# Optimization experiments

Hardware: AMD Instinct MI355X
Metric: run time of the kernel (lower is better)

## Reference

```python
import jax, jax.numpy as jnp
import numpy as np

H = W = 9
C = 16
D = 34
NHEAD = 2
HDIM = D // NHEAD  # 17
FF = 2048
NLAYERS = 2
EPS = 1e-5


def setup_inputs() -> dict:
    key = jax.random.key(0)
    ks = jax.random.split(key, 16)
    s = 0.05
    return {
        "obs": jax.random.normal(ks[0], (2, H, W), dtype=jnp.float32),
        "conv1_w": jax.random.normal(ks[1], (16, 2, 3, 3), dtype=jnp.float32) * s,
        "conv1_b": jnp.zeros((16,), jnp.float32),
        "conv2_w": jax.random.normal(ks[2], (16, 16, 3, 3), dtype=jnp.float32) * s,
        "conv2_b": jnp.zeros((16,), jnp.float32),
        "in_proj_w": jax.random.normal(ks[3], (NLAYERS, 3 * D, D), dtype=jnp.float32) * s,
        "in_proj_b": jnp.zeros((NLAYERS, 3 * D), jnp.float32),
        "out_proj_w": jax.random.normal(ks[4], (NLAYERS, D, D), dtype=jnp.float32) * s,
        "out_proj_b": jnp.zeros((NLAYERS, D), jnp.float32),
        "lin1_w": jax.random.normal(ks[5], (NLAYERS, FF, D), dtype=jnp.float32) * s,
        "lin1_b": jnp.zeros((NLAYERS, FF), jnp.float32),
        "lin2_w": jax.random.normal(ks[6], (NLAYERS, D, FF), dtype=jnp.float32) * s,
        "lin2_b": jnp.zeros((NLAYERS, D), jnp.float32),
        "ln1_g": jnp.ones((NLAYERS, D), jnp.float32),
        "ln1_b": jnp.zeros((NLAYERS, D), jnp.float32),
        "ln2_g": jnp.ones((NLAYERS, D), jnp.float32),
        "ln2_b": jnp.zeros((NLAYERS, D), jnp.float32),
    }


def _layer_norm(x, g, b):
    m = jnp.mean(x, axis=-1, keepdims=True)
    v = jnp.mean(jnp.square(x - m), axis=-1, keepdims=True)
    return (x - m) * jax.lax.rsqrt(v + EPS) * g + b


def _encoder_layer(x, ipw, ipb, opw, opb, l1w, l1b, l2w, l2b, g1, b1, g2, b2):
    # x: [S, D]. Post-norm TransformerEncoderLayer, eval mode (no dropout).
    S = x.shape[0]
    qkv = x @ ipw.T + ipb  # [S, 3D]
    q, k, v = jnp.split(qkv, 3, axis=-1)
    q = q.reshape(S, NHEAD, HDIM).transpose(1, 0, 2)  # [h, S, d]
    k = k.reshape(S, NHEAD, HDIM).transpose(1, 0, 2)
    v = v.reshape(S, NHEAD, HDIM).transpose(1, 0, 2)
    scores = jnp.einsum("hqd,hkd->hqk", q, k) / jnp.sqrt(jnp.float32(HDIM))
    attn = jax.nn.softmax(scores, axis=-1)
    o = jnp.einsum("hqk,hkd->hqd", attn, v)  # [h, S, d]
    o = o.transpose(1, 0, 2).reshape(S, D)
    o = o @ opw.T + opb
    x = _layer_norm(x + o, g1, b1)
    f = jax.nn.relu(x @ l1w.T + l1b) @ l2w.T + l2b
    return _layer_norm(x + f, g2, b2)


def _conv(x, w, b):
    y = jax.lax.conv_general_dilated(
        x, w, window_strides=(1, 1), padding="SAME",
        dimension_numbers=("NCHW", "OIHW", "NCHW"))
    return jax.nn.relu(y + b[None, :, None, None])


def reference(obs, conv1_w, conv1_b, conv2_w, conv2_b, in_proj_w, in_proj_b,
              out_proj_w, out_proj_b, lin1_w, lin1_b, lin2_w, lin2_b,
              ln1_g, ln1_b, ln2_g, ln2_b):
    x = obs[None]  # [1, 2, H, W]
    x = _conv(x, conv1_w, conv1_b)
    x = _conv(x, conv2_w, conv2_b)
    hw = H * W
    cell_emb = x[0].reshape(C, hw).T  # [hw, C]
    idx = jnp.arange(hw)
    r = (idx // W).astype(jnp.float32)
    c = (idx % W).astype(jnp.float32)
    dx = (r[:, None] - r[None, :]) / ((H - 1) / 2.0)  # [hw, hw]
    dy = (c[:, None] - c[None, :]) / ((W - 1) / 2.0)
    tok_i = jnp.broadcast_to(cell_emb[:, None, :], (hw, hw, C))
    tok_j = jnp.broadcast_to(cell_emb[None, :, :], (hw, hw, C))
    rel = jnp.stack([dx, dy], axis=-1)  # [hw, hw, 2]
    tokens = jnp.concatenate([tok_i, tok_j, rel], axis=-1).reshape(hw * hw, D)
    for l in range(NLAYERS):
        tokens = _encoder_layer(
            tokens, in_proj_w[l], in_proj_b[l], out_proj_w[l], out_proj_b[l],
            lin1_w[l], lin1_b[l], lin2_w[l], lin2_b[l],
            ln1_g[l], ln1_b[l], ln2_g[l], ln2_b[l])
    agent_idx = jnp.argmax(obs[0].reshape(-1))
    start = agent_idx * hw
    agent_tokens = jax.lax.dynamic_slice(tokens, (start, 0), (hw, D))
    return agent_tokens.mean(axis=0)  # [D]
```

## Files before the change

kernel.cpp:

```cpp
#include <hip/hip_runtime.h>
#include <hip/hip_bf16.h>

#define HH 9
#define WW 9
#define HW 81
#define CC 16
#define DD 34
#define SS 6561
#define NHEAD 2
#define HD 17
#define FF 2048
#define EPSF 1e-5f

#define NTILES 52
#define QB 64

#define NIP 7168
#define NOP 3072
#define NW1 131072
#define NW2 98304
#define NLTOT (NIP + NOP + NW1 + NW2)
#define LPREP_BLOCKS 1872
#define NKF 425984
#define NVF 212992
#define NV16 13312
#define NOSUM 4608
#define ZERO_WORDS 337408
#define ZERO_BLOCKS 1318

#define NEAB 124416
#define NVFL1 12288
#define KSPLIT 16

typedef __attribute__((ext_vector_type(8))) short bf16x8;
typedef __attribute__((ext_vector_type(4))) float f32x4;

__device__ __forceinline__ unsigned short f2b(float f) {
  unsigned int u = __float_as_uint(f);
  u += 0x7fffu + ((u >> 16) & 1u);
  return (unsigned short)(u >> 16);
}

__global__ __launch_bounds__(256) void prep_kernel(
    const float* __restrict__ obs, const float* __restrict__ w1, const float* __restrict__ b1,
    const float* __restrict__ w2, const float* __restrict__ b2,
    float* __restrict__ cell, int* __restrict__ aidx,
    const float* __restrict__ ipw, const float* __restrict__ opw,
    const float* __restrict__ l1w, const float* __restrict__ l2w,
    unsigned short* __restrict__ ipwp, unsigned short* __restrict__ opwp,
    unsigned short* __restrict__ w1p, unsigned short* __restrict__ w2p,
    unsigned short* __restrict__ kfp, unsigned short* __restrict__ vfp,
    float* __restrict__ v16, float* __restrict__ osum) {
  int bx = blockIdx.x;
  int t = threadIdx.x;
  if (bx == 0) {
    __shared__ float s_obs[2][11][11];
    __shared__ float s_w1[288];
    __shared__ float s_w2[2304];
    __shared__ float s_b1[16], s_b2[16];
    __shared__ float y1[CC][121];
    for (int i = t; i < 2 * 121; i += 256) ((float*)s_obs)[i] = 0.f;
    for (int i = t; i < CC * 121; i += 256) ((float*)y1)[i] = 0.f;
    for (int i = t; i < 288; i += 256) s_w1[i] = w1[i];
    for (int i = t; i < 2304; i += 256) s_w2[i] = w2[i];
    if (t < 16) { s_b1[t] = b1[t]; s_b2[t] = b2[t]; }
    __syncthreads();
    for (int i = t; i < 2 * HW; i += 256) {
      int ic = i / HW, p = i % HW;
      s_obs[ic][1 + p / WW][1 + p % WW] = obs[i];
    }
    __syncthreads();
    if (t == 0) {
      int best = 0; float bv = s_obs[0][1][1];
      for (int p = 1; p < HW; p++) {
        float v = s_obs[0][1 + p / WW][1 + p % WW];
        if (v > bv) { bv = v; best = p; }
      }
      *aidx = best;
    }
    for (int idx = t; idx < CC * HW; idx += 256) {
      int c = idx / HW, p = idx % HW;
      int i = p / WW, j = p % WW;
      float acc = s_b1[c];
#pragma unroll
      for (int ic = 0; ic < 2; ic++)
#pragma unroll
        for (int di = 0; di < 3; di++)
#pragma unroll
          for (int dj = 0; dj < 3; dj++)
            acc += s_obs[ic][i + di][j + dj] * s_w1[((c * 2 + ic) * 3 + di) * 3 + dj];
      y1[c][(i + 1) * 11 + (j + 1)] = fmaxf(acc, 0.f);
    }
    __syncthreads();
    for (int idx = t; idx < CC * HW; idx += 256) {
      int c = idx / HW, p = idx % HW;
      int i = p / WW, j = p % WW;
      float acc = s_b2[c];
#pragma unroll
      for (int ic = 0; ic < CC; ic++)
#pragma unroll
        for (int di = 0; di < 3; di++)
#pragma unroll
          for (int dj = 0; dj < 3; dj++)
            acc += y1[ic][(i + di) * 11 + (j + dj)] * s_w2[((c * CC + ic) * 3 + di) * 3 + dj];
      cell[p * CC + c] = fmaxf(acc, 0.f);
    }
  } else if (bx <= LPREP_BLOCKS) {
    int i = (bx - 1) * 256 + t;
    int layer = i / NLTOT;
    int r = i % NLTOT;
    if (r < NIP) {
      int n = r >> 6, k = r & 63;
      ipwp[layer * NIP + r] =
          (n < 102 && k < DD) ? f2b(ipw[(size_t)layer * 102 * DD + n * DD + k]) : (unsigned short)0;
    } else if (r < NIP + NOP) {
      int rr = r - NIP;
      int n = rr >> 6, k = rr & 63;
      opwp[layer * NOP + rr] =
          (n < DD && k < DD) ? f2b(opw[(size_t)layer * DD * DD + n * DD + k]) : (unsigned short)0;
    } else if (r < NIP + NOP + NW1) {
      int rr = r - NIP - NOP;
      int f = rr >> 6, k = rr & 63;
      w1p[layer * NW1 + rr] =
          (k < DD) ? f2b(l1w[(size_t)layer * FF * DD + f * DD + k]) : (unsigned short)0;
    } else {
      int rr = r - NIP - NOP - NW1;
      int d = rr >> 11, kk = rr & 2047;
      w2p[layer * NW2 + rr] =
          (d < DD) ? f2b(l2w[(size_t)layer * DD * FF + d * FF + kk]) : (unsigned short)0;
    }
  } else {
    int zi = (bx - 1 - LPREP_BLOCKS) * 256 + t;
    if (zi < NKF / 2) ((unsigned int*)kfp)[zi] = 0u;
    else if (zi < NKF / 2 + NVF / 2) ((unsigned int*)vfp)[zi - NKF / 2] = 0u;
    else if (zi < NKF / 2 + NVF / 2 + NV16) v16[zi - NKF / 2 - NVF / 2] = 0.f;
    else if (zi < ZERO_WORDS) osum[zi - NKF / 2 - NVF / 2 - NV16] = 0.f;
  }
}

__global__ __launch_bounds__(256) void ptprep_kernel(
    const float* __restrict__ cell, const float* __restrict__ ipw,
    const float* __restrict__ ipb, float* __restrict__ Pt) {
  int idx = blockIdx.x * 256 + threadIdx.x;
  if (idx >= 2 * HW * 102) return;
  int part = idx / (HW * 102);
  int rem = idx % (HW * 102);
  int a = rem / 102, n = rem % 102;
  float ra = (float)(a / WW) * 0.25f, ca = (float)(a % WW) * 0.25f;
  float acc;
  if (part == 0) {
    acc = ipb[n] + ipw[n * DD + 32] * ra + ipw[n * DD + 33] * ca;
    for (int f = 0; f < CC; f++) acc += ipw[n * DD + f] * cell[a * CC + f];
  } else {
    acc = -(ipw[n * DD + 32] * ra + ipw[n * DD + 33] * ca);
    for (int f = 0; f < CC; f++) acc += ipw[n * DD + CC + f] * cell[a * CC + f];
  }
  Pt[idx] = acc;
}

__global__ __launch_bounds__(256) void expprep_kernel(
    const float* __restrict__ Pt, float* __restrict__ eAB,
    unsigned short* __restrict__ vfragL1) {
  int idx = blockIdx.x * 256 + threadIdx.x;
  const float scale = 0.24253562503633297f;
  if (idx < NEAB) {
    int a = idx % 96; int rest = idx / 96;
    int row = rest % 81; rest /= 81;
    int ab = rest & 1, p = (rest >> 1) & 1, h = rest >> 2;
    float e = 0.f;
    if (a < HW) {
      const float* qrow = Pt + (size_t)ab * (HW * 102) + row * 102 + h * HD;
      const float* krow = Pt + (size_t)p * (HW * 102) + a * 102 + DD + h * HD;
      float dot = 0.f;
#pragma unroll
      for (int d = 0; d < HD; d++) dot += qrow[d] * krow[d];
      e = __expf(fminf(dot * scale, 40.f));
    }
    eAB[idx] = e;
  } else if (idx < NEAB + NVFL1) {
    int j = idx - NEAB;
    int a = j % 96; int rest = j / 96;
    int n = rest % 32; rest /= 32;
    int p = rest & 1, h = rest >> 1;
    float v = 0.f;
    if (a < HW) {
      if (n < HD) v = Pt[(size_t)p * (HW * 102) + a * 102 + 2 * DD + h * HD + n];
      else if (n == HD) v = 1.f;
    }
    vfragL1[((size_t)(h * 2 + p) * 32 + n) * 96 + a] = f2b(v);
  }
}

__global__ __launch_bounds__(256) void fl1_kernel(
    const float* __restrict__ cell, const float* __restrict__ eAB,
    const unsigned short* __restrict__ vfragL1,
    const unsigned short* __restrict__ opwp, const float* __restrict__ opb,
    const float* __restrict__ g1v, const float* __restrict__ b1v,
    const unsigned short* __restrict__ w1p, const unsigned short* __restrict__ w2p,
    const float* __restrict__ fb1, const float* __restrict__ fb2,
    const float* __restrict__ g2v, const float* __restrict__ b2v,
    float* __restrict__ x) {
  __shared__ __align__(16) unsigned short sE[4][16 * 96];
  __shared__ __align__(16) unsigned short soA[16 * 72];
  __shared__ float sxF[16][35];
  __shared__ __align__(16) unsigned short sxA2[16 * 72];
  __shared__ float sxF2[16][35];
  __shared__ __align__(16) unsigned short hw_[4][16 * 40];
  __shared__ float yred[4][16][49];
  int t = threadIdx.x;
  int w = t >> 6, lane = t & 63, quad = lane >> 4, col = lane & 15;
  int r0 = blockIdx.x * 16;
  int nr = min(16, SS - r0);

  for (int i = t; i < 16 * 72; i += 256) { soA[i] = 0; sxA2[i] = 0; }
  for (int i = t; i < 16 * 35; i += 256) { ((float*)sxF)[i] = 0.f; ((float*)sxF2)[i] = 0.f; }
  for (int i = t; i < nr * DD; i += 256) {
    int r = i / DD, d = i - r * DD;
    int row = r0 + r;
    int ii = row / HW, jj = row - ii * HW;
    float v;
    if (d < CC) v = cell[ii * CC + d];
    else if (d < 2 * CC) v = cell[jj * CC + (d - CC)];
    else if (d == 32) v = (float)((ii / WW) - (jj / WW)) * 0.25f;
    else v = (float)((ii % WW) - (jj % WW)) * 0.25f;
    sxF[r][d] = v;
  }

  {
    int h = w >> 1, p = w & 1;
    const float* eA = eAB + ((size_t)((h * 2 + p) * 2 + 0) * 81) * 96;
    const float* eB = eAB + ((size_t)((h * 2 + p) * 2 + 1) * 81) * 96;
    int tl = lane >> 2, asub = lane & 3;
    int row = r0 + tl;
    int tc = row < SS ? row : SS - 1;
    int it = tc / HW, jt = tc - it * HW;
    const float* eAr = eA + it * 96 + asub * 24;
    const float* eBr = eB + jt * 96 + asub * 24;
    unsigned short etmp[24];
#pragma unroll
    for (int k = 0; k < 24; k++) etmp[k] = f2b(eAr[k] * eBr[k]);
    unsigned short* Eb = &sE[w][tl * 96 + asub * 24];
#pragma unroll
    for (int k = 0; k < 3; k++)
      *(bf16x8*)(Eb + k * 8) = *(bf16x8*)(etmp + k * 8);
    const unsigned short* vf = vfragL1 + (size_t)(h * 2 + p) * 32 * 96;
    f32x4 acc0 = {0.f, 0.f, 0.f, 0.f}, acc1 = {0.f, 0.f, 0.f, 0.f};
#pragma unroll
    for (int c = 0; c < 3; c++) {
      bf16x8 ea = *(const bf16x8*)&sE[w][col * 96 + c * 32 + quad * 8];
      bf16x8 vb0 = *(const bf16x8*)&vf[col * 96 + c * 32 + quad * 8];
      bf16x8 vb1 = *(const bf16x8*)&vf[(16 + col) * 96 + c * 32 + quad * 8];
      acc0 = __builtin_amdgcn_mfma_f32_16x16x32_bf16(ea, vb0, acc0, 0, 0, 0);
      acc1 = __builtin_amdgcn_mfma_f32_16x16x32_bf16(ea, vb1, acc1, 0, 0, 0);
    }
    float Sr[4];
#pragma unroll
    for (int r = 0; r < 4; r++) Sr[r] = __shfl(acc1[r], (lane & 48) + 1);
#pragma unroll
    for (int r = 0; r < 4; r++) {
      int rr = quad * 4 + r;
      float inv = 1.f / Sr[r];
      yred[w][rr][col] = acc0[r] * inv;
      if (col == 0) yred[w][rr][16] = acc1[r] * inv;
    }
  }
  __syncthreads();
  for (int i = t; i < 16 * DD; i += 256) {
    int r = i / DD, dd = i - r * DD;
    int h2 = dd / HD, d2 = dd - h2 * HD;
    soA[r * 72 + dd] = f2b(yred[2 * h2][r][d2] + yred[2 * h2 + 1][r][d2]);
  }
  __syncthreads();

  if (w == 0) {
    bf16x8 a0 = *(const bf16x8*)&soA[col * 72 + quad * 8];
    bf16x8 a1 = *(const bf16x8*)&soA[col * 72 + 32 + quad * 8];
    f32x4 y[3];
#pragma unroll
    for (int nt = 0; nt < 3; nt++) {
      int n = nt * 16 + col;
      bf16x8 b0 = *(const bf16x8*)&opwp[n * 64 + quad * 8];
      bf16x8 b1 = *(const bf16x8*)&opwp[n * 64 + 32 + quad * 8];
      f32x4 acc = {0.f, 0.f, 0.f, 0.f};
      acc = __builtin_amdgcn_mfma_f32_16x16x32_bf16(a0, b0, acc, 0, 0, 0);
      y[nt] = __builtin_amdgcn_mfma_f32_16x16x32_bf16(a1, b1, acc, 0, 0, 0);
    }
    float yv[3][4];
    float s1[4] = {0.f, 0.f, 0.f, 0.f}, s2[4] = {0.f, 0.f, 0.f, 0.f};
#pragma unroll
    for (int nt = 0; nt < 3; nt++) {
      int d = nt * 16 + col;
      bool vd = d < DD;
      float ob = vd ? opb[d] : 0.f;
#pragma unroll
      for (int r = 0; r < 4; r++) {
        int row = quad * 4 + r;
        float v = vd ? (y[nt][r] + ob + sxF[row][d]) : 0.f;
        yv[nt][r] = v;
        s1[r] += v;
        s2[r] += v * v;
      }
    }
#pragma unroll
    for (int msk = 1; msk <= 8; msk <<= 1)
#pragma unroll
      for (int r = 0; r < 4; r++) {
        s1[r] += __shfl_xor(s1[r], msk);
        s2[r] += __shfl_xor(s2[r], msk);
      }
#pragma unroll
    for (int r = 0; r < 4; r++) {
      int row = quad * 4 + r;
      float mean = s1[r] * (1.f / DD);
      float var = s2[r] * (1.f / DD) - mean * mean;
      float rs = rsqrtf(var + EPSF);
#pragma unroll
      for (int nt = 0; nt < 3; nt++) {
        int d = nt * 16 + col;
        if (d < DD) {
          float o = (yv[nt][r] - mean) * rs * g1v[d] + b1v[d];
          sxF2[row][d] = o;
          sxA2[row * 72 + d] = f2b(o);
        }
      }
    }
  }
  __syncthreads();

  bf16x8 a0 = *(const bf16x8*)&sxA2[col * 72 + quad * 8];
  bf16x8 a1 = *(const bf16x8*)&sxA2[col * 72 + 32 + quad * 8];
  unsigned short* myh = &hw_[w][0];
  f32x4 acc3[3];
#pragma unroll
  for (int nt = 0; nt < 3; nt++) acc3[nt] = (f32x4){0.f, 0.f, 0.f, 0.f};
  for (int kt = 0; kt < 16; kt++) {
    int fbase = kt * 128 + w * 32;
#pragma unroll
    for (int nt = 0; nt < 2; nt++) {
      int f = fbase + nt * 16 + col;
      bf16x8 b0f = *(const bf16x8*)&w1p[f * 64 + quad * 8];
      bf16x8 b1f = *(const bf16x8*)&w1p[f * 64 + 32 + quad * 8];
      f32x4 hacc = {0.f, 0.f, 0.f, 0.f};
      hacc = __builtin_amdgcn_mfma_f32_16x16x32_bf16(a0, b0f, hacc, 0, 0, 0);
      hacc = __builtin_amdgcn_mfma_f32_16x16x32_bf16(a1, b1f, hacc, 0, 0, 0);
      float bias = fb1[f];
#pragma unroll
      for (int r = 0; r < 4; r++) {
        float hv = fmaxf(hacc[r] + bias, 0.f);
        myh[(quad * 4 + r) * 40 + nt * 16 + col] = f2b(hv);
      }
    }
    bf16x8 pa = *(const bf16x8*)&myh[col * 40 + quad * 8];
#pragma unroll
    for (int nt = 0; nt < 3; nt++) {
      int n = nt * 16 + col;
      bf16x8 wb = *(const bf16x8*)&w2p[(size_t)n * FF + fbase + quad * 8];
      acc3[nt] = __builtin_amdgcn_mfma_f32_16x16x32_bf16(pa, wb, acc3[nt], 0, 0, 0);
    }
  }
#pragma unroll
  for (int nt = 0; nt < 3; nt++)
#pragma unroll
    for (int r = 0; r < 4; r++)
      yred[w][quad * 4 + r][nt * 16 + col] = acc3[nt][r];
  __syncthreads();
  if (w == 0) {
    float yv[3][4];
    float s1[4] = {0.f, 0.f, 0.f, 0.f}, s2[4] = {0.f, 0.f, 0.f, 0.f};
#pragma unroll
    for (int nt = 0; nt < 3; nt++) {
      int d = nt * 16 + col;
      bool valid = d < DD;
      float b2x = valid ? fb2[d] : 0.f;
#pragma unroll
      for (int r = 0; r < 4; r++) {
        int row = quad * 4 + r;
        float v = yred[0][row][nt * 16 + col] + yred[1][row][nt * 16 + col]
                + yred[2][row][nt * 16 + col] + yred[3][row][nt * 16 + col];
        v = valid ? (v + b2x + sxF2[row][d]) : 0.f;
        yv[nt][r] = v;
        s1[r] += v;
        s2[r] += v * v;
      }
    }
#pragma unroll
    for (int msk = 1; msk <= 8; msk <<= 1)
#pragma unroll
      for (int r = 0; r < 4; r++) {
        s1[r] += __shfl_xor(s1[r], msk);
        s2[r] += __shfl_xor(s2[r], msk);
      }
#pragma unroll
    for (int r = 0; r < 4; r++) {
      int row = quad * 4 + r;
      if (row >= nr) continue;
      float mean = s1[r] * (1.f / DD);
      float var = s2[r] * (1.f / DD) - mean * mean;
      float rs = rsqrtf(var + EPSF);
#pragma unroll
      for (int nt = 0; nt < 3; nt++) {
        int d = nt * 16 + col;
        if (d < DD)
          x[(size_t)(r0 + row) * DD + d] = (yv[nt][r] - mean) * rs * g2v[d] + b2v[d];
      }
    }
  }
}

__global__ __launch_bounds__(256) void qkv2_kernel(
    const float* __restrict__ x, const unsigned short* __restrict__ ipwp,
    const float* __restrict__ ipb, const int* __restrict__ abase,
    float* __restrict__ qkv, unsigned short* __restrict__ kfp,
    unsigned short* __restrict__ vfp, float* __restrict__ v16) {
  __shared__ __align__(16) unsigned short sxA[16 * 72];
  int t = threadIdx.x;
  int w = t >> 6, lane = t & 63, quad = lane >> 4, col = lane & 15;
  bool qpart = blockIdx.x >= 411;
  int row0 = qpart ? (abase[0] * HW + (blockIdx.x - 411) * 16) : blockIdx.x * 16;
  int nr = min(16, SS - row0);
  for (int i = t; i < 16 * 72; i += 256) sxA[i] = 0;
  __syncthreads();
  for (int i = t; i < nr * DD; i += 256) {
    int r = i / DD, d = i - r * DD;
    sxA[r * 72 + d] = f2b(x[(size_t)(row0 + r) * DD + d]);
  }
  __syncthreads();
  bf16x8 a0 = *(const bf16x8*)&sxA[col * 72 + quad * 8];
  bf16x8 a1 = *(const bf16x8*)&sxA[col * 72 + 32 + quad * 8];
  if (!qpart) {
    int npass = (w == 0) ? 2 : 1;
    for (int pass = 0; pass < npass; pass++) {
      int nt = (pass == 0) ? w : 4;
      int n = DD + nt * 16 + col;
      int nc = n < 112 ? n : 111;
      bf16x8 b0 = *(const bf16x8*)&ipwp[nc * 64 + quad * 8];
      bf16x8 b1 = *(const bf16x8*)&ipwp[nc * 64 + 32 + quad * 8];
      f32x4 acc = {0.f, 0.f, 0.f, 0.f};
      acc = __builtin_amdgcn_mfma_f32_16x16x32_bf16(a0, b0, acc, 0, 0, 0);
      acc = __builtin_amdgcn_mfma_f32_16x16x32_bf16(a1, b1, acc, 0, 0, 0);
      if (n < 102) {
        float bias = ipb[n];
        int kd = n - DD;
#pragma unroll
        for (int r = 0; r < 4; r++) {
          int m = quad * 4 + r;
          if (m >= nr) continue;
          int tok = row0 + m;
          float val = acc[r] + bias;
          int T = tok >> 7, tl = tok & 127;
          if (kd < 2 * HD) {
            int h = kd >= HD;
            int d = kd - h * HD;
            int colf = tl >> 3, ntk = tl & 7;
            kfp[(((size_t)h * NTILES + T) * 8 + ntk) * 512 +
                ((d >> 3) * 16 + colf) * 8 + (d & 7)] = f2b(val);
          } else {
            int vd = kd - 2 * HD;
            int h = vd >= HD;
            int d = vd - h * HD;
            if (d < 16) {
              int c = tl >> 5, qf = (tl >> 3) & 3, j = tl & 7;
              vfp[(((size_t)h * NTILES + T) * 4 + c) * 512 +
                  (qf * 16 + d) * 8 + j] = f2b(val);
            } else {
              v16[(size_t)h * (NTILES * 128) + tok] = val;
            }
          }
        }
      }
    }
  } else {
    if (w < 3) {
      int n = w * 16 + col;
      bf16x8 b0 = *(const bf16x8*)&ipwp[n * 64 + quad * 8];
      bf16x8 b1 = *(const bf16x8*)&ipwp[n * 64 + 32 + quad * 8];
      f32x4 acc = {0.f, 0.f, 0.f, 0.f};
      acc = __builtin_amdgcn_mfma_f32_16x16x32_bf16(a0, b0, acc, 0, 0, 0);
      acc = __builtin_amdgcn_mfma_f32_16x16x32_bf16(a1, b1, acc, 0, 0, 0);
      if (n < DD) {
        float bias = ipb[n];
#pragma unroll
        for (int r = 0; r < 4; r++) {
          int m = row0 + quad * 4 + r;
          if (m < SS) qkv[(size_t)m * 102 + n] = acc[r] + bias;
        }
      }
    }
  }
}

__global__ __launch_bounds__(256) void attn2_kernel(
    const float* __restrict__ qkv, const unsigned short* __restrict__ kfp,
    const unsigned short* __restrict__ vfp, const float* __restrict__ v16,
    const int* __restrict__ abase, float* __restrict__ o_sum, float* __restrict__ l_sum) {
  __shared__ __align__(16) unsigned short scb[4][16 * 136];
  int t = threadIdx.x, w = t >> 6, lane = t & 63, quad = lane >> 4, col = lane & 15;
  int h = blockIdx.y;
  int tile = blockIdx.z;
  int base = abase[0] * HW;
  int q0 = blockIdx.x * QB;
  const float scale = 0.24253562503633297f;
  const unsigned short* kf = kfp + (size_t)h * (NTILES * 8 * 512);
  const unsigned short* vf = vfp + (size_t)h * (NTILES * 4 * 512);
  const float* v16h = v16 + (size_t)h * (NTILES * 128);
  unsigned short* myscb = &scb[w][0];

  int mq = base + q0 + w * 16 + col;
  int qc = mq < SS ? mq : SS - 1;
  bf16x8 aq;
#pragma unroll
  for (int j = 0; j < 8; j++) {
    int d = quad * 8 + j;
    aq[j] = (short)((d < HD) ? f2b(qkv[(size_t)qc * 102 + h * HD + d] * scale) : 0);
  }

  int k0 = tile * 128;
  const unsigned short* kt = kf + (size_t)tile * (8 * 512);
  f32x4 s[8];
#pragma unroll
  for (int nt = 0; nt < 8; nt++) {
    bf16x8 kb = *(const bf16x8*)(kt + nt * 512 + lane * 8);
    f32x4 z = {0.f, 0.f, 0.f, 0.f};
    s[nt] = __builtin_amdgcn_mfma_f32_16x16x32_bf16(aq, kb, z, 0, 0, 0);
  }
  if (k0 + 128 > SS) {
#pragma unroll
    for (int nt = 0; nt < 8; nt++)
      if (k0 + col * 8 + nt >= SS) {
        s[nt][0] = -1e30f; s[nt][1] = -1e30f; s[nt][2] = -1e30f; s[nt][3] = -1e30f;
      }
  }
  float lreg[4];
#pragma unroll
  for (int r = 0; r < 4; r++) {
    bf16x8 pv;
    float psl = 0.f;
#pragma unroll
    for (int nt = 0; nt < 8; nt++) {
      float p = __expf(fminf(s[nt][r], 70.f));
      s[nt][r] = p;
      psl += p;
      pv[nt] = (short)f2b(p);
    }
    lreg[r] = psl;
    *(bf16x8*)(myscb + (quad * 4 + r) * 136 + col * 8) = pv;
  }
  float o16a[4];
  f32x4 va = *(const f32x4*)(v16h + k0 + col * 8);
  f32x4 vb4 = *(const f32x4*)(v16h + k0 + col * 8 + 4);
#pragma unroll
  for (int r = 0; r < 4; r++) {
    o16a[r] = s[0][r] * va[0] + s[1][r] * va[1] + s[2][r] * va[2] + s[3][r] * va[3]
            + s[4][r] * vb4[0] + s[5][r] * vb4[1] + s[6][r] * vb4[2] + s[7][r] * vb4[3];
  }
  f32x4 oacc = {0.f, 0.f, 0.f, 0.f};
  const unsigned short* vt = vf + (size_t)tile * (4 * 512);
#pragma unroll
  for (int c = 0; c < 4; c++) {
    bf16x8 pa = *(const bf16x8*)(myscb + col * 136 + c * 32 + quad * 8);
    bf16x8 vbf = *(const bf16x8*)(vt + c * 512 + lane * 8);
    oacc = __builtin_amdgcn_mfma_f32_16x16x32_bf16(pa, vbf, oacc, 0, 0, 0);
  }
#pragma unroll
  for (int msk = 1; msk <= 8; msk <<= 1)
#pragma unroll
    for (int r = 0; r < 4; r++) {
      o16a[r] += __shfl_xor(o16a[r], msk);
      lreg[r] += __shfl_xor(lreg[r], msk);
    }
#pragma unroll
  for (int r = 0; r < 4; r++) {
    int ql = q0 + w * 16 + quad * 4 + r;
    if (ql < HW) {
      atomicAdd(&o_sum[(size_t)ql * DD + h * HD + col], oacc[r]);
      if (col == 0) {
        atomicAdd(&o_sum[(size_t)ql * DD + h * HD + 16], o16a[r]);
        atomicAdd(&l_sum[h * 128 + ql], lreg[r]);
      }
    }
  }
}

__global__ __launch_bounds__(256) void fl2a_kernel(
    const float* __restrict__ o_sum, const float* __restrict__ l_sum,
    const unsigned short* __restrict__ opwp, const float* __restrict__ opb,
    const float* __restrict__ g1v, const float* __restrict__ b1v,
    const unsigned short* __restrict__ w1p, const unsigned short* __restrict__ w2p,
    const float* __restrict__ fb1, const int* __restrict__ abase,
    const float* __restrict__ x, float* __restrict__ xln, float* __restrict__ ypart) {
  __shared__ __align__(16) unsigned short soA[16 * 72];
  __shared__ float sxF[16][35];
  __shared__ __align__(16) unsigned short sxA2[16 * 72];
  __shared__ __align__(16) unsigned short hw_[4][16 * 40];
  __shared__ float yred[4][16][49];
  int t = threadIdx.x;
  int w = t >> 6, lane = t & 63, quad = lane >> 4, col = lane & 15;
  int sp = blockIdx.y;
  int base = abase[0] * HW;
  int ql0 = blockIdx.x * 16;
  int nr = min(16, HW - ql0);
  int r0 = base + ql0;

  for (int i = t; i < 16 * 72; i += 256) { soA[i] = 0; sxA2[i] = 0; }
  for (int i = t; i < 16 * 35; i += 256) ((float*)sxF)[i] = 0.f;
  __syncthreads();
  for (int i = t; i < nr * DD; i += 256) {
    int r = i / DD, rem = i - r * DD;
    sxF[r][rem] = x[(size_t)(r0 + r) * DD + rem];
    int ql = ql0 + r;
    int h = rem / HD;
    float L = l_sum[h * 128 + ql];
    float O = o_sum[(size_t)ql * DD + rem];
    soA[r * 72 + rem] = f2b(O / L);
  }
  __syncthreads();
  if (w == 0) {
    bf16x8 a0 = *(const bf16x8*)&soA[col * 72 + quad * 8];
    bf16x8 a1 = *(const bf16x8*)&soA[col * 72 + 32 + quad * 8];
    f32x4 y[3];
#pragma unroll
    for (int nt = 0; nt < 3; nt++) {
      int n = nt * 16 + col;
      bf16x8 b0 = *(const bf16x8*)&opwp[n * 64 + quad * 8];
      bf16x8 b1 = *(const bf16x8*)&opwp[n * 64 + 32 + quad * 8];
      f32x4 acc = {0.f, 0.f, 0.f, 0.f};
      acc = __builtin_amdgcn_mfma_f32_16x16x32_bf16(a0, b0, acc, 0, 0, 0);
      y[nt] = __builtin_amdgcn_mfma_f32_16x16x32_bf16(a1, b1, acc, 0, 0, 0);
    }
    float yv[3][4];
    float s1[4] = {0.f, 0.f, 0.f, 0.f}, s2[4] = {0.f, 0.f, 0.f, 0.f};
#pragma unroll
    for (int nt = 0; nt < 3; nt++) {
      int d = nt * 16 + col;
      bool vd = d < DD;
      float ob = vd ? opb[d] : 0.f;
#pragma unroll
      for (int r = 0; r < 4; r++) {
        int row = quad * 4 + r;
        float v = vd ? (y[nt][r] + ob + sxF[row][d]) : 0.f;
        yv[nt][r] = v;
        s1[r] += v;
        s2[r] += v * v;
      }
    }
#pragma unroll
    for (int msk = 1; msk <= 8; msk <<= 1)
#pragma unroll
      for (int r = 0; r < 4; r++) {
        s1[r] += __shfl_xor(s1[r], msk);
        s2[r] += __shfl_xor(s2[r], msk);
      }
#pragma unroll
    for (int r = 0; r < 4; r++) {
      int row = quad * 4 + r;
      float mean = s1[r] * (1.f / DD);
      float var = s2[r] * (1.f / DD) - mean * mean;
      float rs = rsqrtf(var + EPSF);
#pragma unroll
      for (int nt = 0; nt < 3; nt++) {
        int d = nt * 16 + col;
        if (d < DD) {
          float o = (yv[nt][r] - mean) * rs * g1v[d] + b1v[d];
          sxA2[row * 72 + d] = f2b(o);
          if (sp == 0 && row < nr)
            xln[(size_t)(ql0 + row) * DD + d] = o;
        }
      }
    }
  }
  __syncthreads();
  bf16x8 a0 = *(const bf16x8*)&sxA2[col * 72 + quad * 8];
  bf16x8 a1 = *(const bf16x8*)&sxA2[col * 72 + 32 + quad * 8];
  unsigned short* myh = &hw_[w][0];
  f32x4 acc3[3];
#pragma unroll
  for (int nt = 0; nt < 3; nt++) acc3[nt] = (f32x4){0.f, 0.f, 0.f, 0.f};
  {
    int fbase = sp * 128 + w * 32;
#pragma unroll
    for (int nt = 0; nt < 2; nt++) {
      int f = fbase + nt * 16 + col;
      bf16x8 b0f = *(const bf16x8*)&w1p[f * 64 + quad * 8];
      bf16x8 b1f = *(const bf16x8*)&w1p[f * 64 + 32 + quad * 8];
      f32x4 hacc = {0.f, 0.f, 0.f, 0.f};
      hacc = __builtin_amdgcn_mfma_f32_16x16x32_bf16(a0, b0f, hacc, 0, 0, 0);
      hacc = __builtin_amdgcn_mfma_f32_16x16x32_bf16(a1, b1f, hacc, 0, 0, 0);
      float bias = fb1[f];
#pragma unroll
      for (int r = 0; r < 4; r++) {
        float hv = fmaxf(hacc[r] + bias, 0.f);
        myh[(quad * 4 + r) * 40 + nt * 16 + col] = f2b(hv);
      }
    }
    bf16x8 pa = *(const bf16x8*)&myh[col * 40 + quad * 8];
#pragma unroll
    for (int nt = 0; nt < 3; nt++) {
      int n = nt * 16 + col;
      bf16x8 wb = *(const bf16x8*)&w2p[(size_t)n * FF + fbase + quad * 8];
      acc3[nt] = __builtin_amdgcn_mfma_f32_16x16x32_bf16(pa, wb, acc3[nt], 0, 0, 0);
    }
  }
#pragma unroll
  for (int nt = 0; nt < 3; nt++)
#pragma unroll
    for (int r = 0; r < 4; r++)
      yred[w][quad * 4 + r][nt * 16 + col] = acc3[nt][r];
  __syncthreads();
  if (w == 0) {
    for (int i = lane; i < nr * DD; i += 64) {
      int r = i / DD, d = i - r * DD;
      float v = yred[0][r][d] + yred[1][r][d] + yred[2][r][d] + yred[3][r][d];
      ypart[((size_t)sp * HW + ql0 + r) * DD + d] = v;
    }
  }
}

__global__ __launch_bounds__(256) void fl2b_kernel(
    const float* __restrict__ ypart, const float* __restrict__ xln,
    const float* __restrict__ fb2, const float* __restrict__ g2v,
    const float* __restrict__ b2v, const int* __restrict__ abase,
    float* __restrict__ x) {
  int t = threadIdx.x;
  int row = blockIdx.x * 32 + (t >> 3);
  int s8 = t & 7;
  if (row >= HW) return;
  int base = abase[0] * HW;
  float yv[5];
  float s1 = 0.f, s2 = 0.f;
  int cnt = 0;
  for (int d = s8; d < DD; d += 8) {
    float v = fb2[d] + xln[(size_t)row * DD + d];
#pragma unroll
    for (int sp = 0; sp < KSPLIT; sp++)
      v += ypart[((size_t)sp * HW + row) * DD + d];
    yv[cnt++] = v;
    s1 += v;
    s2 += v * v;
  }
  s1 += __shfl_xor(s1, 1); s2 += __shfl_xor(s2, 1);
  s1 += __shfl_xor(s1, 2); s2 += __shfl_xor(s2, 2);
  s1 += __shfl_xor(s1, 4); s2 += __shfl_xor(s2, 4);
  float mean = s1 * (1.f / DD);
  float var = s2 * (1.f / DD) - mean * mean;
  float rs = rsqrtf(var + EPSF);
  cnt = 0;
  for (int d = s8; d < DD; d += 8)
    x[(size_t)(base + row) * DD + d] = (yv[cnt++] - mean) * rs * g2v[d] + b2v[d];
}

__global__ __launch_bounds__(64) void final_kernel(
    const float* __restrict__ x, const int* __restrict__ aidx, float* __restrict__ out) {
  int d = threadIdx.x;
  if (d >= DD) return;
  int start = (*aidx) * HW;
  float acc = 0.f;
  for (int j = 0; j < HW; j++) acc += x[(size_t)(start + j) * DD + d];
  out[d] = acc * (1.f / HW);
}

extern "C" void kernel_launch(void* const* d_in, const int* in_sizes, int n_in,
                              void* d_out, int out_size, void* d_ws, size_t ws_size,
                              hipStream_t stream) {
  const float* obs = (const float*)d_in[0];
  const float* c1w = (const float*)d_in[1];
  const float* c1b = (const float*)d_in[2];
  const float* c2w = (const float*)d_in[3];
  const float* c2b = (const float*)d_in[4];
  const float* ipw = (const float*)d_in[5];
  const float* ipb = (const float*)d_in[6];
  const float* opw = (const float*)d_in[7];
  const float* opb = (const float*)d_in[8];
  const float* l1w = (const float*)d_in[9];
  const float* l1b = (const float*)d_in[10];
  const float* l2w = (const float*)d_in[11];
  const float* l2b = (const float*)d_in[12];
  const float* g1 = (const float*)d_in[13];
  const float* b1 = (const float*)d_in[14];
  const float* g2 = (const float*)d_in[15];
  const float* b2 = (const float*)d_in[16];
  float* out = (float*)d_out;

  float* ws = (float*)d_ws;
  size_t off = 0;
  float* x     = ws + off; off += SS * DD;
  float* qkv   = ws + off; off += SS * 102;
  float* cell  = ws + off; off += HW * CC;
  int*   aidx  = (int*)(ws + off); off += 1;
  off = (off + 3) & ~(size_t)3;
  float* Pt    = ws + off; off += 2 * HW * 102;
  float* eAB   = ws + off; off += NEAB;
  float* xln   = ws + off; off += HW * DD;
  float* ypart = ws + off; off += (size_t)KSPLIT * HW * DD;
  off = (off + 3) & ~(size_t)3;
  unsigned short* vfragL1 = (unsigned short*)(ws + off); off += NVFL1 / 2;
  unsigned short* kfp  = (unsigned short*)(ws + off); off += NKF / 2;
  unsigned short* vfp  = (unsigned short*)(ws + off); off += NVF / 2;
  float* v16 = ws + off; off += NV16;
  float* o_sum = ws + off; off += 128 * DD;
  float* l_sum = ws + off; off += 256;
  unsigned short* ipwp = (unsigned short*)(ws + off); off += 2 * NIP / 2;
  unsigned short* opwp = (unsigned short*)(ws + off); off += 2 * NOP / 2;
  unsigned short* w1p  = (unsigned short*)(ws + off); off += 2 * NW1 / 2;
  unsigned short* w2p  = (unsigned short*)(ws + off); off += 2 * NW2 / 2;

  const int prep_grid = 1 + LPREP_BLOCKS + ZERO_BLOCKS;
  const int pt_blocks = (2 * HW * 102 + 255) / 256;
  const int exp_blocks = (NEAB + NVFL1 + 255) / 256;
  const int fl1_blocks = (SS + 15) / 16;

  prep_kernel<<<prep_grid, 256, 0, stream>>>(
      obs, c1w, c1b, c2w, c2b, cell, aidx,
      ipw, opw, l1w, l2w, ipwp, opwp, w1p, w2p, kfp, vfp, v16, o_sum);
  ptprep_kernel<<<pt_blocks, 256, 0, stream>>>(cell, ipw, ipb, Pt);
  expprep_kernel<<<exp_blocks, 256, 0, stream>>>(Pt, eAB, vfragL1);
  fl1_kernel<<<fl1_blocks, 256, 0, stream>>>(
      cell, eAB, vfragL1, opwp, opb, g1, b1, w1p, w2p, l1b, l2b, g2, b2, x);
  qkv2_kernel<<<419, 256, 0, stream>>>(
      x, ipwp + NIP, ipb + 102, aidx, qkv, kfp, vfp, v16);
  dim3 a2g(2, NHEAD, NTILES);
  attn2_kernel<<<a2g, 256, 0, stream>>>(qkv, kfp, vfp, v16, aidx, o_sum, l_sum);
  dim3 f2g(6, KSPLIT);
  fl2a_kernel<<<f2g, 256, 0, stream>>>(
      o_sum, l_sum, opwp + NOP, opb + DD, g1 + DD, b1 + DD,
      w1p + NW1, w2p + NW2, l1b + FF, aidx, x, xln, ypart);
  fl2b_kernel<<<3, 256, 0, stream>>>(
      ypart, xln, l2b + DD, g2 + DD, b2 + DD, aidx, x);
  final_kernel<<<1, 64, 0, stream>>>(x, aidx, out);
}
```

Baseline: 181.7 us.

## Fuse projection prep kernels, fold layer-2 QKV into FFN kernel, atomic final mean

Merges the Pt and exp/V-fragment prep kernels into one 12-block kernel that computes per-head Q/K/V projections in shared memory. The layer-2 QKV projection is now done inside the layer-1 FFN kernel, straight from the bf16 LN output in shared memory, so x is no longer re-read and one launch goes away. The final mean kernel is replaced by atomic adds in fl2b, with the output zeroed in prep. This removes three launches and a global round trip, but the prep now runs on only 12 blocks, fl1 grows in register and work load, and the atomics make the summation order nondeterministic.

```diff
diff --git a/kernel.cpp b/kernel.cpp
--- a/kernel.cpp
+++ b/kernel.cpp
@@ -50,7 +50,7 @@
     unsigned short* __restrict__ ipwp, unsigned short* __restrict__ opwp,
     unsigned short* __restrict__ w1p, unsigned short* __restrict__ w2p,
     unsigned short* __restrict__ kfp, unsigned short* __restrict__ vfp,
-    float* __restrict__ v16, float* __restrict__ osum) {
+    float* __restrict__ v16, float* __restrict__ osum, float* __restrict__ outp) {
   int bx = blockIdx.x;
   int t = threadIdx.x;
   if (bx == 0) {
@@ -130,6 +130,7 @@
           (d < DD) ? f2b(l2w[(size_t)layer * DD * FF + d * FF + kk]) : (unsigned short)0;
     }
   } else {
+    if (bx == LPREP_BLOCKS + 1 && t < DD) outp[t] = 0.f;
     int zi = (bx - 1 - LPREP_BLOCKS) * 256 + t;
     if (zi < NKF / 2) ((unsigned int*)kfp)[zi] = 0u;
     else if (zi < NKF / 2 + NVF / 2) ((unsigned int*)vfp)[zi - NKF / 2] = 0u;
@@ -138,56 +139,73 @@
   }
 }
 
-__global__ __launch_bounds__(256) void ptprep_kernel(
+__global__ __launch_bounds__(256) void eprep_kernel(
     const float* __restrict__ cell, const float* __restrict__ ipw,
-    const float* __restrict__ ipb, float* __restrict__ Pt) {
-  int idx = blockIdx.x * 256 + threadIdx.x;
-  if (idx >= 2 * HW * 102) return;
-  int part = idx / (HW * 102);
-  int rem = idx % (HW * 102);
-  int a = rem / 102, n = rem % 102;
-  float ra = (float)(a / WW) * 0.25f, ca = (float)(a % WW) * 0.25f;
-  float acc;
-  if (part == 0) {
-    acc = ipb[n] + ipw[n * DD + 32] * ra + ipw[n * DD + 33] * ca;
-    for (int f = 0; f < CC; f++) acc += ipw[n * DD + f] * cell[a * CC + f];
+    const float* __restrict__ ipb, float* __restrict__ eAB,
+    unsigned short* __restrict__ vfragL1) {
+  __shared__ float qr[81][17];
+  __shared__ float kr[81][17];
+  int bx = blockIdx.x, t = threadIdx.x;
+  const float scale = 0.24253562503633297f;
+  if (bx < 8) {
+    int ab = bx & 1, p = (bx >> 1) & 1, h = (bx >> 2) & 1;
+    for (int i = t; i < 2 * 81 * 17; i += 256) {
+      int side = i / (81 * 17);
+      int rem = i - side * 81 * 17;
+      int a = rem / 17, d = rem - a * 17;
+      int part = side == 0 ? ab : p;
+      int n = (side == 0 ? 0 : DD) + h * HD + d;
+      float ra = (float)(a / WW) * 0.25f, ca = (float)(a % WW) * 0.25f;
+      float acc;
+      if (part == 0) {
+        acc = ipb[n] + ipw[n * DD + 32] * ra + ipw[n * DD + 33] * ca;
+        for (int f = 0; f < CC; f++) acc += ipw[n * DD + f] * cell[a * CC + f];
+      } else {
+        acc = -(ipw[n * DD + 32] * ra + ipw[n * DD + 33] * ca);
+        for (int f = 0; f < CC; f++) acc += ipw[n * DD + CC + f] * cell[a * CC + f];
+      }
+      if (side == 0) qr[a][d] = acc; else kr[a][d] = acc;
+    }
+    __syncthreads();
+    float* base = eAB + ((size_t)((h * 2 + p) * 2 + ab) * 81) * 96;
+    for (int i = t; i < 81 * 96; i += 256) {
+      int row = i / 96, a = i - row * 96;
+      float e = 0.f;
+      if (a < HW) {
+        float dot = 0.f;
+#pragma unroll
+        for (int d = 0; d < HD; d++) dot += qr[row][d] * kr[a][d];
+        e = __expf(fminf(dot * scale, 40.f));
+      }
+      base[row * 96 + a] = e;
+    }
   } else {
-    acc = -(ipw[n * DD + 32] * ra + ipw[n * DD + 33] * ca);
-    for (int f = 0; f < CC; f++) acc += ipw[n * DD + CC + f] * cell[a * CC + f];
-  }
-  Pt[idx] = acc;
-}
-
-__global__ __launch_bounds__(256) void expprep_kernel(
-    const float* __restrict__ Pt, float* __restrict__ eAB,
-    unsigned short* __restrict__ vfragL1) {
-  int idx = blockIdx.x * 256 + threadIdx.x;
-  const float scale = 0.24253562503633297f;
-  if (idx < NEAB) {
-    int a = idx % 96; int rest = idx / 96;
-    int row = rest % 81; rest /= 81;
-    int ab = rest & 1, p = (rest >> 1) & 1, h = rest >> 2;
-    float e = 0.f;
-    if (a < HW) {
-      const float* qrow = Pt + (size_t)ab * (HW * 102) + row * 102 + h * HD;
-      const float* krow = Pt + (size_t)p * (HW * 102) + a * 102 + DD + h * HD;
-      float dot = 0.f;
-#pragma unroll
-      for (int d = 0; d < HD; d++) dot += qrow[d] * krow[d];
-      e = __expf(fminf(dot * scale, 40.f));
-    }
-    eAB[idx] = e;
-  } else if (idx < NEAB + NVFL1) {
-    int j = idx - NEAB;
-    int a = j % 96; int rest = j / 96;
-    int n = rest % 32; rest /= 32;
-    int p = rest & 1, h = rest >> 1;
-    float v = 0.f;
-    if (a < HW) {
-      if (n < HD) v = Pt[(size_t)p * (HW * 102) + a * 102 + 2 * DD + h * HD + n];
-      else if (n == HD) v = 1.f;
-    }
-    vfragL1[((size_t)(h * 2 + p) * 32 + n) * 96 + a] = f2b(v);
+    int hp = bx - 8;
+    int h = hp >> 1, p = hp & 1;
+    for (int i = t; i < 81 * 17; i += 256) {
+      int a = i / 17, d = i - a * 17;
+      int n = 2 * DD + h * HD + d;
+      float ra = (float)(a / WW) * 0.25f, ca = (float)(a % WW) * 0.25f;
+      float acc;
+      if (p == 0) {
+        acc = ipb[n] + ipw[n * DD + 32] * ra + ipw[n * DD + 33] * ca;
+        for (int f = 0; f < CC; f++) acc += ipw[n * DD + f] * cell[a * CC + f];
+      } else {
+        acc = -(ipw[n * DD + 32] * ra + ipw[n * DD + 33] * ca);
+        for (int f = 0; f < CC; f++) acc += ipw[n * DD + CC + f] * cell[a * CC + f];
+      }
+      qr[a][d] = acc;
+    }
+    __syncthreads();
+    for (int i = t; i < 32 * 96; i += 256) {
+      int n = i / 96, a = i - n * 96;
+      float v = 0.f;
+      if (a < HW) {
+        if (n < HD) v = qr[a][n];
+        else if (n == HD) v = 1.f;
+      }
+      vfragL1[((size_t)(h * 2 + p) * 32 + n) * 96 + a] = f2b(v);
+    }
   }
 }
 
@@ -199,7 +217,10 @@
     const unsigned short* __restrict__ w1p, const unsigned short* __restrict__ w2p,
     const float* __restrict__ fb1, const float* __restrict__ fb2,
     const float* __restrict__ g2v, const float* __restrict__ b2v,
-    float* __restrict__ x) {
+    const unsigned short* __restrict__ ipwp2, const float* __restrict__ ipb2,
+    const int* __restrict__ abase, float* __restrict__ x, float* __restrict__ qkv,
+    unsigned short* __restrict__ kfp, unsigned short* __restrict__ vfp,
+    float* __restrict__ v16) {
   __shared__ __align__(16) unsigned short sE[4][16 * 96];
   __shared__ __align__(16) unsigned short soA[16 * 72];
   __shared__ float sxF[16][35];
@@ -393,59 +414,44 @@
 #pragma unroll
     for (int r = 0; r < 4; r++) {
       int row = quad * 4 + r;
-      if (row >= nr) continue;
       float mean = s1[r] * (1.f / DD);
       float var = s2[r] * (1.f / DD) - mean * mean;
       float rs = rsqrtf(var + EPSF);
 #pragma unroll
       for (int nt = 0; nt < 3; nt++) {
         int d = nt * 16 + col;
-        if (d < DD)
-          x[(size_t)(r0 + row) * DD + d] = (yv[nt][r] - mean) * rs * g2v[d] + b2v[d];
-      }
-    }
-  }
-}
-
-__global__ __launch_bounds__(256) void qkv2_kernel(
-    const float* __restrict__ x, const unsigned short* __restrict__ ipwp,
-    const float* __restrict__ ipb, const int* __restrict__ abase,
-    float* __restrict__ qkv, unsigned short* __restrict__ kfp,
-    unsigned short* __restrict__ vfp, float* __restrict__ v16) {
-  __shared__ __align__(16) unsigned short sxA[16 * 72];
-  int t = threadIdx.x;
-  int w = t >> 6, lane = t & 63, quad = lane >> 4, col = lane & 15;
-  bool qpart = blockIdx.x >= 411;
-  int row0 = qpart ? (abase[0] * HW + (blockIdx.x - 411) * 16) : blockIdx.x * 16;
-  int nr = min(16, SS - row0);
-  for (int i = t; i < 16 * 72; i += 256) sxA[i] = 0;
+        if (d < DD) {
+          float xv = (yv[nt][r] - mean) * rs * g2v[d] + b2v[d];
+          soA[row * 72 + d] = f2b(xv);
+          if (row < nr) x[(size_t)(r0 + row) * DD + d] = xv;
+        }
+      }
+    }
+  }
   __syncthreads();
-  for (int i = t; i < nr * DD; i += 256) {
-    int r = i / DD, d = i - r * DD;
-    sxA[r * 72 + d] = f2b(x[(size_t)(row0 + r) * DD + d]);
-  }
-  __syncthreads();
-  bf16x8 a0 = *(const bf16x8*)&sxA[col * 72 + quad * 8];
-  bf16x8 a1 = *(const bf16x8*)&sxA[col * 72 + 32 + quad * 8];
-  if (!qpart) {
+
+  {
+    bf16x8 xa0 = *(const bf16x8*)&soA[col * 72 + quad * 8];
+    bf16x8 xa1 = *(const bf16x8*)&soA[col * 72 + 32 + quad * 8];
+    int base = abase[0] * HW;
     int npass = (w == 0) ? 2 : 1;
     for (int pass = 0; pass < npass; pass++) {
       int nt = (pass == 0) ? w : 4;
       int n = DD + nt * 16 + col;
       int nc = n < 112 ? n : 111;
-      bf16x8 b0 = *(const bf16x8*)&ipwp[nc * 64 + quad * 8];
-      bf16x8 b1 = *(const bf16x8*)&ipwp[nc * 64 + 32 + quad * 8];
+      bf16x8 b0 = *(const bf16x8*)&ipwp2[nc * 64 + quad * 8];
+      bf16x8 b1 = *(const bf16x8*)&ipwp2[nc * 64 + 32 + quad * 8];
       f32x4 acc = {0.f, 0.f, 0.f, 0.f};
-      acc = __builtin_amdgcn_mfma_f32_16x16x32_bf16(a0, b0, acc, 0, 0, 0);
-      acc = __builtin_amdgcn_mfma_f32_16x16x32_bf16(a1, b1, acc, 0, 0, 0);
+      acc = __builtin_amdgcn_mfma_f32_16x16x32_bf16(xa0, b0, acc, 0, 0, 0);
+      acc = __builtin_amdgcn_mfma_f32_16x16x32_bf16(xa1, b1, acc, 0, 0, 0);
       if (n < 102) {
-        float bias = ipb[n];
+        float bias = ipb2[n];
         int kd = n - DD;
 #pragma unroll
         for (int r = 0; r < 4; r++) {
           int m = quad * 4 + r;
           if (m >= nr) continue;
-          int tok = row0 + m;
+          int tok = r0 + m;
           float val = acc[r] + bias;
           int T = tok >> 7, tl = tok & 127;
           if (kd < 2 * HD) {
@@ -469,20 +475,21 @@
         }
       }
     }
-  } else {
-    if (w < 3) {
+    if (r0 + 16 > base && r0 < base + 128 && w < 3) {
       int n = w * 16 + col;
-      bf16x8 b0 = *(const bf16x8*)&ipwp[n * 64 + quad * 8];
-      bf16x8 b1 = *(const bf16x8*)&ipwp[n * 64 + 32 + quad * 8];
+      bf16x8 b0 = *(const bf16x8*)&ipwp2[n * 64 + quad * 8];
+      bf16x8 b1 = *(const bf16x8*)&ipwp2[n * 64 + 32 + quad * 8];
       f32x4 acc = {0.f, 0.f, 0.f, 0.f};
-      acc = __builtin_amdgcn_mfma_f32_16x16x32_bf16(a0, b0, acc, 0, 0, 0);
-      acc = __builtin_amdgcn_mfma_f32_16x16x32_bf16(a1, b1, acc, 0, 0, 0);
+      acc = __builtin_amdgcn_mfma_f32_16x16x32_bf16(xa0, b0, acc, 0, 0, 0);
+      acc = __builtin_amdgcn_mfma_f32_16x16x32_bf16(xa1, b1, acc, 0, 0, 0);
       if (n < DD) {
-        float bias = ipb[n];
+        float bias = ipb2[n];
 #pragma unroll
         for (int r = 0; r < 4; r++) {
-          int m = row0 + quad * 4 + r;
-          if (m < SS) qkv[(size_t)m * 102 + n] = acc[r] + bias;
+          int m = quad * 4 + r;
+          int row = r0 + m;
+          if (m < nr && row >= base && row < base + 128)
+            qkv[(size_t)row * 102 + n] = acc[r] + bias;
         }
       }
     }
@@ -718,13 +725,11 @@
 __global__ __launch_bounds__(256) void fl2b_kernel(
     const float* __restrict__ ypart, const float* __restrict__ xln,
     const float* __restrict__ fb2, const float* __restrict__ g2v,
-    const float* __restrict__ b2v, const int* __restrict__ abase,
-    float* __restrict__ x) {
+    const float* __restrict__ b2v, float* __restrict__ out) {
   int t = threadIdx.x;
   int row = blockIdx.x * 32 + (t >> 3);
   int s8 = t & 7;
   if (row >= HW) return;
-  int base = abase[0] * HW;
   float yv[5];
   float s1 = 0.f, s2 = 0.f;
   int cnt = 0;
@@ -744,18 +749,10 @@
   float var = s2 * (1.f / DD) - mean * mean;
   float rs = rsqrtf(var + EPSF);
   cnt = 0;
-  for (int d = s8; d < DD; d += 8)
-    x[(size_t)(base + row) * DD + d] = (yv[cnt++] - mean) * rs * g2v[d] + b2v[d];
-}
-
-__global__ __launch_bounds__(64) void final_kernel(
-    const float* __restrict__ x, const int* __restrict__ aidx, float* __restrict__ out) {
-  int d = threadIdx.x;
-  if (d >= DD) return;
-  int start = (*aidx) * HW;
-  float acc = 0.f;
-  for (int j = 0; j < HW; j++) acc += x[(size_t)(start + j) * DD + d];
-  out[d] = acc * (1.f / HW);
+  for (int d = s8; d < DD; d += 8) {
+    float xv = (yv[cnt++] - mean) * rs * g2v[d] + b2v[d];
+    atomicAdd(&out[d], xv * (1.f / HW));
+  }
 }
 
 extern "C" void kernel_launch(void* const* d_in, const int* in_sizes, int n_in,
@@ -787,7 +784,6 @@
   float* cell  = ws + off; off += HW * CC;
   int*   aidx  = (int*)(ws + off); off += 1;
   off = (off + 3) & ~(size_t)3;
-  float* Pt    = ws + off; off += 2 * HW * 102;
   float* eAB   = ws + off; off += NEAB;
   float* xln   = ws + off; off += HW * DD;
   float* ypart = ws + off; off += (size_t)KSPLIT * HW * DD;
@@ -804,19 +800,15 @@
   unsigned short* w2p  = (unsigned short*)(ws + off); off += 2 * NW2 / 2;
 
   const int prep_grid = 1 + LPREP_BLOCKS + ZERO_BLOCKS;
-  const int pt_blocks = (2 * HW * 102 + 255) / 256;
-  const int exp_blocks = (NEAB + NVFL1 + 255) / 256;
   const int fl1_blocks = (SS + 15) / 16;
 
   prep_kernel<<<prep_grid, 256, 0, stream>>>(
       obs, c1w, c1b, c2w, c2b, cell, aidx,
-      ipw, opw, l1w, l2w, ipwp, opwp, w1p, w2p, kfp, vfp, v16, o_sum);
-  ptprep_kernel<<<pt_blocks, 256, 0, stream>>>(cell, ipw, ipb, Pt);
-  expprep_kernel<<<exp_blocks, 256, 0, stream>>>(Pt, eAB, vfragL1);
+      ipw, opw, l1w, l2w, ipwp, opwp, w1p, w2p, kfp, vfp, v16, o_sum, out);
+  eprep_kernel<<<12, 256, 0, stream>>>(cell, ipw, ipb, eAB, vfragL1);
   fl1_kernel<<<fl1_blocks, 256, 0, stream>>>(
-      cell, eAB, vfragL1, opwp, opb, g1, b1, w1p, w2p, l1b, l2b, g2, b2, x);
-  qkv2_kernel<<<419, 256, 0, stream>>>(
-      x, ipwp + NIP, ipb + 102, aidx, qkv, kfp, vfp, v16);
+      cell, eAB, vfragL1, opwp, opb, g1, b1, w1p, w2p, l1b, l2b, g2, b2,
+      ipwp + NIP, ipb + 102, aidx, x, qkv, kfp, vfp, v16);
   dim3 a2g(2, NHEAD, NTILES);
   attn2_kernel<<<a2g, 256, 0, stream>>>(qkv, kfp, vfp, v16, aidx, o_sum, l_sum);
   dim3 f2g(6, KSPLIT);
@@ -824,6 +816,5 @@
       o_sum, l_sum, opwp + NOP, opb + DD, g1 + DD, b1 + DD,
       w1p + NW1, w2p + NW2, l1b + FF, aidx, x, xln, ypart);
   fl2b_kernel<<<3, 256, 0, stream>>>(
-      ypart, xln, l2b + DD, g2 + DD, b2 + DD, aidx, x);
-  final_kernel<<<1, 64, 0, stream>>>(x, aidx, out);
+      ypart, xln, l2b + DD, g2 + DD, b2 + DD, out);
 }
```

Measured after the change: 192.5 us. 1.06x slower.
